# Optimization experiments

Measured on AMD Instinct MI355X. Metric: run time of the kernel, lower is better.

The kernel has to match this reference:

```python
import jax, jax.numpy as jnp
import numpy as np

SIZES = {"a": 1024, "b": 512, "c": 2048}
OUT = 1024
N_STREAMS = 3
EPS = 1e-5


def _layer_norm(x, w, b):
    mu = jnp.mean(x, axis=-1, keepdims=True)
    var = jnp.mean(jnp.square(x - mu), axis=-1, keepdims=True)
    return (x - mu) * jax.lax.rsqrt(var + EPS) * w + b


def setup_inputs() -> dict:
    key = jax.random.key(0)
    ks = iter(jax.random.split(key, 32))
    B = 32768
    inp = {}
    for name, d in SIZES.items():
        inp[f"x_{name}"] = jax.random.normal(next(ks), (B, d), dtype=jnp.float32)
        inp[f"ln_w_{name}"] = jnp.ones((d,), dtype=jnp.float32)
        inp[f"ln_b_{name}"] = jnp.zeros((d,), dtype=jnp.float32)
        inp[f"W_{name}"] = jax.random.normal(next(ks), (d, OUT), dtype=jnp.float32) / np.sqrt(d)
        inp[f"b_{name}"] = jnp.zeros((OUT,), dtype=jnp.float32)
        # gating linear: size -> n_streams * gate_size (gate_size = OUT, pointwise)
        inp[f"Wg_{name}"] = 0.005 * jax.random.normal(next(ks), (d, N_STREAMS * OUT), dtype=jnp.float32)
        inp[f"bg_{name}"] = jnp.zeros((N_STREAMS * OUT,), dtype=jnp.float32)
    return inp


def reference(x_a, ln_w_a, ln_b_a, W_a, b_a, Wg_a, bg_a,
              x_b, ln_w_b, ln_b_b, W_b, b_b, Wg_b, bg_b,
              x_c, ln_w_c, ln_b_c, W_c, b_c, Wg_c, bg_c):
    xs = [x_a, x_b, x_c]
    lns = [(ln_w_a, ln_b_a), (ln_w_b, ln_b_b), (ln_w_c, ln_b_c)]
    lins = [(W_a, b_a), (W_b, b_b), (W_c, b_c)]
    gats = [(Wg_a, bg_a), (Wg_b, bg_b), (Wg_c, bg_c)]

    gate_logits = 0.0
    outputs = []
    for x, (lw, lb), (W, b), (Wg, bg) in zip(xs, lns, lins, gats):
        f = jax.nn.relu(_layer_norm(x, lw, lb))          # [B, d]
        outputs.append(f @ W + b)                         # [B, OUT]
        gate_logits = gate_logits + (f @ Wg + bg)         # [B, 3*OUT]

    B = x_a.shape[0]
    gate = jax.nn.softmax(gate_logits.reshape(B, N_STREAMS, OUT), axis=1)  # [B,3,OUT]
    out = sum(gate[:, i] * outputs[i] for i in range(N_STREAMS))
    return out
```

## Files before the change

kernel.cpp:

```cpp
#include <hip/hip_runtime.h>
#include <hip/hip_bf16.h>
#include <stdint.h>

#define B_ROWS 32768
#define KTOT   3584
#define NC     6144
#define OUT_N  1024

typedef unsigned short ushort_t;
typedef __attribute__((ext_vector_type(8))) short bf16x8;
typedef __attribute__((ext_vector_type(4))) float f32x4;

__device__ __forceinline__ float b2f(unsigned short u) {
    union { unsigned int i; float f; } x; x.i = ((unsigned int)u) << 16; return x.f;
}
__device__ __forceinline__ unsigned short f2b(float f) {
    union { float f; unsigned int i; } x; x.f = f;
    unsigned int r = x.i + 0x7fffu + ((x.i >> 16) & 1u);
    return (unsigned short)(r >> 16);
}

__device__ __forceinline__ void gload_lds16(const void* g, void* l) {
    auto g1 = reinterpret_cast<const __attribute__((address_space(1))) char*>(
        reinterpret_cast<uintptr_t>(g));
    auto l3 = reinterpret_cast<__attribute__((address_space(3))) char*>(
        (uint32_t)reinterpret_cast<uintptr_t>(l));
    __builtin_amdgcn_global_load_lds(g1, l3, 16, 0, 0);
}

template<int OFF>
__device__ __forceinline__ bf16x8 dsr(uint32_t addr) {
    bf16x8 d;
    asm volatile("ds_read_b128 %0, %1 offset:%2" : "=v"(d) : "v"(addr), "i"(OFF));
    return d;
}

__global__ __launch_bounds__(256) void pack_wt_kernel(
    const float* __restrict__ Wa, const float* __restrict__ Wga,
    const float* __restrict__ Wb, const float* __restrict__ Wgb,
    const float* __restrict__ Wc, const float* __restrict__ Wgc,
    ushort_t* __restrict__ WT)
{
    int s = blockIdx.y;
    const float *Ws, *Wgs; int d, koff;
    if (s == 0)      { Ws = Wa; Wgs = Wga; d = 1024; koff = 0;    }
    else if (s == 1) { Ws = Wb; Wgs = Wgb; d = 512;  koff = 1024; }
    else             { Ws = Wc; Wgs = Wgc; d = 2048; koff = 1536; }
    int kt = blockIdx.x >> 6;
    int ntile = blockIdx.x & 63;
    if (kt >= (d >> 6)) return;
    int k0 = kt * 64, n0 = ntile * 64;
    const float* src; int ld, ncol0;
    if (n0 < 1024) { src = Ws;  ld = 1024; ncol0 = n0; }
    else           { src = Wgs; ld = 3072; ncol0 = n0 - 1024; }

    __shared__ float tile[64][65];
    int tx = threadIdx.x & 63, ty = threadIdx.x >> 6;
    for (int r = ty; r < 64; r += 4)
        tile[r][tx] = src[(size_t)(k0 + r) * ld + ncol0 + tx];
    __syncthreads();
    for (int r = ty; r < 64; r += 4)
        WT[(size_t)(n0 + r) * KTOT + koff + k0 + tx] = f2b(tile[tx][r]);
}

__global__ __launch_bounds__(256) void pack_bias_kernel(
    const float* __restrict__ ba, const float* __restrict__ bb, const float* __restrict__ bc,
    const float* __restrict__ bga, const float* __restrict__ bgb, const float* __restrict__ bgc,
    float* __restrict__ bias)
{
    int i = blockIdx.x * 256 + threadIdx.x;
    if (i >= NC) return;
    float v;
    if (i < 1024)      v = ba[i];
    else if (i < 2048) v = bb[i - 1024];
    else if (i < 3072) v = bc[i - 2048];
    else { int g = i - 3072; v = bga[g] + bgb[g] + bgc[g]; }
    bias[i] = v;
}

__global__ __launch_bounds__(256) void ln_relu_kernel(
    const float* __restrict__ xa, const float* __restrict__ xb, const float* __restrict__ xc,
    const float* __restrict__ wa, const float* __restrict__ wb, const float* __restrict__ wc,
    const float* __restrict__ ba, const float* __restrict__ bb, const float* __restrict__ bc,
    ushort_t* __restrict__ F)
{
    int row = blockIdx.x;
    int s = blockIdx.y;
    const float *x, *w, *b; int d, koff;
    if (s == 0)      { x = xa; w = wa; b = ba; d = 1024; koff = 0;    }
    else if (s == 1) { x = xb; w = wb; b = bb; d = 512;  koff = 1024; }
    else             { x = xc; w = wc; b = bc; d = 2048; koff = 1536; }
    const float* xr = x + (size_t)row * d;
    int tid = threadIdx.x;

    float s1 = 0.f, s2 = 0.f;
    for (int i = tid * 4; i < d; i += 1024) {
        float4 v = *(const float4*)(xr + i);
        s1 += v.x + v.y + v.z + v.w;
        s2 += v.x * v.x + v.y * v.y + v.z * v.z + v.w * v.w;
    }
    for (int o = 32; o > 0; o >>= 1) {
        s1 += __shfl_down(s1, o, 64);
        s2 += __shfl_down(s2, o, 64);
    }
    __shared__ float red1[4], red2[4], bcast[2];
    int wv = tid >> 6, ln = tid & 63;
    if (ln == 0) { red1[wv] = s1; red2[wv] = s2; }
    __syncthreads();
    if (tid == 0) {
        float t1 = red1[0] + red1[1] + red1[2] + red1[3];
        float t2 = red2[0] + red2[1] + red2[2] + red2[3];
        float mean = t1 / d;
        float var = t2 / d - mean * mean;
        bcast[0] = mean;
        bcast[1] = rsqrtf(var + 1e-5f);
    }
    __syncthreads();
    float mean = bcast[0], rstd = bcast[1];

    ushort_t* Fr = F + (size_t)row * KTOT + koff;
    for (int i = tid * 4; i < d; i += 1024) {
        float4 v  = *(const float4*)(xr + i);
        float4 wv4 = *(const float4*)(w + i);
        float4 bv4 = *(const float4*)(b + i);
        float o0 = fmaxf(0.f, (v.x - mean) * rstd * wv4.x + bv4.x);
        float o1 = fmaxf(0.f, (v.y - mean) * rstd * wv4.y + bv4.y);
        float o2 = fmaxf(0.f, (v.z - mean) * rstd * wv4.z + bv4.z);
        float o3 = fmaxf(0.f, (v.w - mean) * rstd * wv4.w + bv4.w);
        union { ushort_t u[4]; uint2 v2; } pk;
        pk.u[0] = f2b(o0); pk.u[1] = f2b(o1); pk.u[2] = f2b(o2); pk.u[3] = f2b(o3);
        *(uint2*)(Fr + i) = pk.v2;
    }
}

__global__ __launch_bounds__(512, 2) void gemm_kernel(
    const ushort_t* __restrict__ F, const ushort_t* __restrict__ WT,
    const float* __restrict__ bias, ushort_t* __restrict__ C)
{
    extern __shared__ ushort_t lds_u16[];

    int bid = blockIdx.x;
    int newid = (bid & 7) * 384 + (bid >> 3);
    int rowpanel = newid / 24;
    int j = newid % 24;
    int row0 = rowpanel * 256;
    int n0, koff, klen, c0;
    if (j < 4)       { n0 = j * 256;            koff = 0;    klen = 1024; c0 = j * 256; }
    else if (j < 8)  { n0 = (j - 4) * 256;      koff = 1024; klen = 512;  c0 = 1024 + (j - 4) * 256; }
    else if (j < 12) { n0 = (j - 8) * 256;      koff = 1536; klen = 2048; c0 = 2048 + (j - 8) * 256; }
    else             { n0 = 1024 + (j - 12) * 256; koff = 0; klen = 3584; c0 = 3072 + (j - 12) * 256; }

    int tid = threadIdx.x, w = tid >> 6, l = tid & 63;
    int wm0 = (w >> 2) * 128;
    int wn0 = (w & 3) * 64;

    int srow = w * 32 + (l >> 3);
    int scol = (((l & 7) ^ (l >> 3)) << 3);
    const ushort_t* Ag = F  + (size_t)(row0 + srow) * KTOT + koff + scol;
    const ushort_t* Bg = WT + (size_t)(n0   + srow) * KTOT + koff + scol;

    uint32_t lds_base = (uint32_t)(uintptr_t)lds_u16;
    uint32_t ldsStA = lds_base + (uint32_t)w * 4096u;

#define STG_A(SELOFF, kt, JJ0) do {                                              \
        gload_lds16(Ag + (size_t)(kt) * 64 + (size_t)(JJ0) * 8 * KTOT,           \
                    (void*)(uintptr_t)(ldsStA + (SELOFF) + (JJ0) * 1024u));      \
        gload_lds16(Ag + (size_t)(kt) * 64 + (size_t)((JJ0) + 1) * 8 * KTOT,     \
                    (void*)(uintptr_t)(ldsStA + (SELOFF) + ((JJ0) + 1) * 1024u)); } while (0)
#define STG_B(SELOFF, kt, JJ0) do {                                              \
        gload_lds16(Bg + (size_t)(kt) * 64 + (size_t)(JJ0) * 8 * KTOT,           \
                    (void*)(uintptr_t)(ldsStA + 32768u + (SELOFF) + (JJ0) * 1024u)); \
        gload_lds16(Bg + (size_t)(kt) * 64 + (size_t)((JJ0) + 1) * 8 * KTOT,     \
                    (void*)(uintptr_t)(ldsStA + 32768u + (SELOFF) + ((JJ0) + 1) * 1024u)); } while (0)

    int rl = l & 15;
    int c16_0 = ((l >> 4)    ) ^ (l & 7);
    int c16_1 = ((l >> 4) + 4) ^ (l & 7);
    uint32_t aA0 = lds_base + (uint32_t)((wm0 + rl) * 128 + c16_0 * 16);
    uint32_t aA1 = lds_base + (uint32_t)((wm0 + rl) * 128 + c16_1 * 16);
    uint32_t aB0 = lds_base + 32768u + (uint32_t)((wn0 + rl) * 128 + c16_0 * 16);
    uint32_t aB1 = lds_base + 32768u + (uint32_t)((wn0 + rl) * 128 + c16_1 * 16);

#define R_A4(dst, base, MI0) do {                          \
        dst[0] = dsr<((MI0)+0)*2048>(base);                \
        dst[1] = dsr<((MI0)+1)*2048>(base);                \
        dst[2] = dsr<((MI0)+2)*2048>(base);                \
        dst[3] = dsr<((MI0)+3)*2048>(base); } while (0)
#define R_B2(dst, base, NI0) do {                          \
        dst[0] = dsr<((NI0)+0)*2048>(base);                \
        dst[1] = dsr<((NI0)+1)*2048>(base); } while (0)

#define MFMA_Q(Aks0, Aks1, Bks0, Bks1, MI0, NI0) do {                            \
        _Pragma("unroll")                                                        \
        for (int mi = 0; mi < 4; ++mi)                                           \
            _Pragma("unroll")                                                    \
            for (int ni = 0; ni < 2; ++ni)                                       \
                acc[(MI0)+mi][(NI0)+ni] = __builtin_amdgcn_mfma_f32_16x16x32_bf16( \
                    Aks0[mi], Bks0[ni], acc[(MI0)+mi][(NI0)+ni], 0, 0, 0);       \
        _Pragma("unroll")                                                        \
        for (int mi = 0; mi < 4; ++mi)                                           \
            _Pragma("unroll")                                                    \
            for (int ni = 0; ni < 2; ++ni)                                       \
                acc[(MI0)+mi][(NI0)+ni] = __builtin_amdgcn_mfma_f32_16x16x32_bf16( \
                    Aks1[mi], Bks1[ni], acc[(MI0)+mi][(NI0)+ni], 0, 0, 0);       \
        } while (0)

    f32x4 acc[8][4];
    #pragma unroll
    for (int mi = 0; mi < 8; ++mi)
        #pragma unroll
        for (int ni = 0; ni < 4; ++ni)
            acc[mi][ni] = (f32x4){0.f, 0.f, 0.f, 0.f};

    int nkt = klen >> 6;

    STG_A(0u, 0, 0); STG_A(0u, 0, 2); STG_B(0u, 0, 0); STG_B(0u, 0, 2);
    STG_A(65536u, 1, 0);

    for (int t = 0; t < nkt; ++t) {
        const uint32_t co  = (t & 1) ? 65536u : 0u;
        const uint32_t no_ = co ^ 65536u;
        int t1 = (t + 1 < nkt) ? t + 1 : nkt - 1;
        int t2 = (t + 2 < nkt) ? t + 2 : nkt - 1;

        asm volatile("s_waitcnt vmcnt(2)" ::: "memory");
        __builtin_amdgcn_s_barrier();

        bf16x8 alo0[4], alo1[4], ahi0[4], ahi1[4];
        bf16x8 blo0[2], blo1[2], bhi0[2], bhi1[2];

        R_A4(alo0, aA0 + co, 0); R_A4(alo1, aA1 + co, 0);
        R_B2(blo0, aB0 + co, 0); R_B2(blo1, aB1 + co, 0);
        STG_A(no_, t1, 2);
        __builtin_amdgcn_s_barrier();
        asm volatile("s_waitcnt lgkmcnt(0)" ::: "memory");
        __builtin_amdgcn_sched_barrier(0);
        __builtin_amdgcn_s_setprio(1);
        MFMA_Q(alo0, alo1, blo0, blo1, 0, 0);
        __builtin_amdgcn_s_setprio(0);
        __builtin_amdgcn_s_barrier();

        R_B2(bhi0, aB0 + co, 2); R_B2(bhi1, aB1 + co, 2);
        STG_B(no_, t1, 0);
        __builtin_amdgcn_s_barrier();
        asm volatile("s_waitcnt lgkmcnt(0)" ::: "memory");
        __builtin_amdgcn_sched_barrier(0);
        __builtin_amdgcn_s_setprio(1);
        MFMA_Q(alo0, alo1, bhi0, bhi1, 0, 2);
        __builtin_amdgcn_s_setprio(0);
        __builtin_amdgcn_s_barrier();

        R_A4(ahi0, aA0 + co, 4); R_A4(ahi1, aA1 + co, 4);
        STG_B(no_, t1, 2);
        __builtin_amdgcn_s_barrier();
        asm volatile("s_waitcnt lgkmcnt(0)" ::: "memory");
        __builtin_amdgcn_sched_barrier(0);
        __builtin_amdgcn_s_setprio(1);
        MFMA_Q(ahi0, ahi1, blo0, blo1, 4, 0);
        __builtin_amdgcn_s_setprio(0);
        __builtin_amdgcn_s_barrier();

        STG_A(co, t2, 0);
        __builtin_amdgcn_s_barrier();
        __builtin_amdgcn_s_setprio(1);
        MFMA_Q(ahi0, ahi1, bhi0, bhi1, 4, 2);
        __builtin_amdgcn_s_setprio(0);
    }

#undef STG_A
#undef STG_B
#undef R_A4
#undef R_B2
#undef MFMA_Q

    #pragma unroll
    for (int ni = 0; ni < 4; ++ni) {
        int col = c0 + wn0 + ni * 16 + rl;
        float bv = bias[col];
        #pragma unroll
        for (int mi = 0; mi < 8; ++mi) {
            int rbase = row0 + wm0 + mi * 16 + (l >> 4) * 4;
            #pragma unroll
            for (int r = 0; r < 4; ++r)
                C[(size_t)(rbase + r) * NC + col] = f2b(acc[mi][ni][r] + bv);
        }
    }
}

typedef __attribute__((ext_vector_type(8))) unsigned short u16x8;

__global__ __launch_bounds__(256) void fuse_kernel(
    const ushort_t* __restrict__ C, float* __restrict__ out)
{
    int t = blockIdx.x * 256 + threadIdx.x;
    int b  = t >> 7;
    int j0 = (t & 127) << 3;
    const ushort_t* Cr = C + (size_t)b * NC;
    u16x8 oa = *(const u16x8*)(Cr + j0);
    u16x8 ob = *(const u16x8*)(Cr + 1024 + j0);
    u16x8 oc = *(const u16x8*)(Cr + 2048 + j0);
    u16x8 g0 = *(const u16x8*)(Cr + 3072 + j0);
    u16x8 g1 = *(const u16x8*)(Cr + 4096 + j0);
    u16x8 g2 = *(const u16x8*)(Cr + 5120 + j0);
    float res[8];
    #pragma unroll
    for (int k = 0; k < 8; ++k) {
        float a0 = b2f(g0[k]), a1 = b2f(g1[k]), a2 = b2f(g2[k]);
        float m = fmaxf(a0, fmaxf(a1, a2));
        float e0 = __expf(a0 - m), e1 = __expf(a1 - m), e2 = __expf(a2 - m);
        float inv = 1.f / (e0 + e1 + e2);
        res[k] = (e0 * b2f(oa[k]) + e1 * b2f(ob[k]) + e2 * b2f(oc[k])) * inv;
    }
    float* op = out + (size_t)b * 1024 + j0;
    *(float4*)op       = (float4){res[0], res[1], res[2], res[3]};
    *(float4*)(op + 4) = (float4){res[4], res[5], res[6], res[7]};
}

extern "C" void kernel_launch(void* const* d_in, const int* in_sizes, int n_in,
                              void* d_out, int out_size, void* d_ws, size_t ws_size,
                              hipStream_t stream)
{
    const float* x_a   = (const float*)d_in[0];
    const float* lnw_a = (const float*)d_in[1];
    const float* lnb_a = (const float*)d_in[2];
    const float* W_a   = (const float*)d_in[3];
    const float* b_a   = (const float*)d_in[4];
    const float* Wg_a  = (const float*)d_in[5];
    const float* bg_a  = (const float*)d_in[6];
    const float* x_b   = (const float*)d_in[7];
    const float* lnw_b = (const float*)d_in[8];
    const float* lnb_b = (const float*)d_in[9];
    const float* W_b   = (const float*)d_in[10];
    const float* b_b   = (const float*)d_in[11];
    const float* Wg_b  = (const float*)d_in[12];
    const float* bg_b  = (const float*)d_in[13];
    const float* x_c   = (const float*)d_in[14];
    const float* lnw_c = (const float*)d_in[15];
    const float* lnb_c = (const float*)d_in[16];
    const float* W_c   = (const float*)d_in[17];
    const float* b_c   = (const float*)d_in[18];
    const float* Wg_c  = (const float*)d_in[19];
    const float* bg_c  = (const float*)d_in[20];

    char* ws = (char*)d_ws;
    ushort_t* F    = (ushort_t*)ws;
    ushort_t* WT   = (ushort_t*)(ws + 234881024);
    ushort_t* Cbuf = (ushort_t*)(ws + 234881024 + 29360128);
    float*    bias = (float*)   (ws + 234881024 + 29360128 + 402653184);

    hipLaunchKernelGGL(pack_wt_kernel, dim3(2048, 3), dim3(256), 0, stream,
                       W_a, Wg_a, W_b, Wg_b, W_c, Wg_c, WT);
    hipLaunchKernelGGL(pack_bias_kernel, dim3(24), dim3(256), 0, stream,
                       b_a, b_b, b_c, bg_a, bg_b, bg_c, bias);
    hipLaunchKernelGGL(ln_relu_kernel, dim3(32768, 3), dim3(256), 0, stream,
                       x_a, x_b, x_c, lnw_a, lnw_b, lnw_c, lnb_a, lnb_b, lnb_c, F);
    hipLaunchKernelGGL(gemm_kernel, dim3(3072), dim3(512), 131072, stream,
                       F, WT, bias, Cbuf);
    hipLaunchKernelGGL(fuse_kernel, dim3(16384), dim3(256), 0, stream,
                       Cbuf, (float*)d_out);
}
```

Before: 1.081 ms.

## Restructure GEMM main loop into one-barrier double buffer with interleaved LDS reads

Replaces the four-phase per-iteration schedule, which had many block barriers and staggered partial prefetches, with a simpler double-buffer scheme. The whole next K tile is issued at the top of each iteration and there is a single vmcnt(0) plus barrier at the end. LDS fragment reads are interleaved with MFMA groups using graded lgkmcnt waits, so compute can start before all fragments arrive. It also changes the block-to-tile mapping so each XCD handles a fixed set of column tiles across row panels, aiming for better L2 reuse of weights. In exchange the global-load prefetch distance drops to one tile, and the full vmcnt(0) wait each iteration may expose memory latency.

```diff
diff --git a/kernel.cpp b/kernel.cpp
--- a/kernel.cpp
+++ b/kernel.cpp
@@ -140,10 +140,15 @@
     extern __shared__ ushort_t lds_u16[];
 
     int bid = blockIdx.x;
-    int newid = (bid & 7) * 384 + (bid >> 3);
-    int rowpanel = newid / 24;
-    int j = newid % 24;
-    int row0 = rowpanel * 256;
+    int xcd = bid & 7;
+    int local = bid >> 3;
+    int rp = local / 3;
+    int jj = local - rp * 3;
+    int j;
+    if (xcd < 4) j = (jj == 0) ? xcd : (jj == 1) ? 8 + xcd : 12 + xcd;
+    else         j = (jj == 0) ? xcd : (jj == 1) ? 12 + xcd : 16 + xcd;
+
+    int row0 = rp * 256;
     int n0, koff, klen, c0;
     if (j < 4)       { n0 = j * 256;            koff = 0;    klen = 1024; c0 = j * 256; }
     else if (j < 8)  { n0 = (j - 4) * 256;      koff = 1024; klen = 512;  c0 = 1024 + (j - 4) * 256; }
@@ -181,29 +186,19 @@
     uint32_t aB0 = lds_base + 32768u + (uint32_t)((wn0 + rl) * 128 + c16_0 * 16);
     uint32_t aB1 = lds_base + 32768u + (uint32_t)((wn0 + rl) * 128 + c16_1 * 16);
 
-#define R_A4(dst, base, MI0) do {                          \
-        dst[0] = dsr<((MI0)+0)*2048>(base);                \
-        dst[1] = dsr<((MI0)+1)*2048>(base);                \
-        dst[2] = dsr<((MI0)+2)*2048>(base);                \
-        dst[3] = dsr<((MI0)+3)*2048>(base); } while (0)
-#define R_B2(dst, base, NI0) do {                          \
-        dst[0] = dsr<((NI0)+0)*2048>(base);                \
-        dst[1] = dsr<((NI0)+1)*2048>(base); } while (0)
-
-#define MFMA_Q(Aks0, Aks1, Bks0, Bks1, MI0, NI0) do {                            \
-        _Pragma("unroll")                                                        \
-        for (int mi = 0; mi < 4; ++mi)                                           \
-            _Pragma("unroll")                                                    \
-            for (int ni = 0; ni < 2; ++ni)                                       \
+#define WAITL(N) do { asm volatile("s_waitcnt lgkmcnt(" #N ")" ::: "memory");   \
+                      __builtin_amdgcn_sched_barrier(0); } while (0)
+
+#define MFMA8(AV, BV, MI0, NI0) do {                                            \
+        __builtin_amdgcn_s_setprio(1);                                          \
+        _Pragma("unroll")                                                       \
+        for (int mi = 0; mi < 4; ++mi)                                          \
+            _Pragma("unroll")                                                   \
+            for (int ni = 0; ni < 2; ++ni)                                      \
                 acc[(MI0)+mi][(NI0)+ni] = __builtin_amdgcn_mfma_f32_16x16x32_bf16( \
-                    Aks0[mi], Bks0[ni], acc[(MI0)+mi][(NI0)+ni], 0, 0, 0);       \
-        _Pragma("unroll")                                                        \
-        for (int mi = 0; mi < 4; ++mi)                                           \
-            _Pragma("unroll")                                                    \
-            for (int ni = 0; ni < 2; ++ni)                                       \
-                acc[(MI0)+mi][(NI0)+ni] = __builtin_amdgcn_mfma_f32_16x16x32_bf16( \
-                    Aks1[mi], Bks1[ni], acc[(MI0)+mi][(NI0)+ni], 0, 0, 0);       \
-        } while (0)
+                    AV[mi], BV[ni], acc[(MI0)+mi][(NI0)+ni], 0, 0, 0);          \
+        __builtin_amdgcn_s_setprio(0);                                          \
+    } while (0)
 
     f32x4 acc[8][4];
     #pragma unroll
@@ -215,63 +210,65 @@
     int nkt = klen >> 6;
 
     STG_A(0u, 0, 0); STG_A(0u, 0, 2); STG_B(0u, 0, 0); STG_B(0u, 0, 2);
-    STG_A(65536u, 1, 0);
+    asm volatile("s_waitcnt vmcnt(0)" ::: "memory");
+    __builtin_amdgcn_s_barrier();
 
     for (int t = 0; t < nkt; ++t) {
         const uint32_t co  = (t & 1) ? 65536u : 0u;
         const uint32_t no_ = co ^ 65536u;
-        int t1 = (t + 1 < nkt) ? t + 1 : nkt - 1;
-        int t2 = (t + 2 < nkt) ? t + 2 : nkt - 1;
-
-        asm volatile("s_waitcnt vmcnt(2)" ::: "memory");
-        __builtin_amdgcn_s_barrier();
+        uint32_t A0 = aA0 + co, A1 = aA1 + co, B0 = aB0 + co, B1 = aB1 + co;
+
+        if (t + 1 < nkt) {
+            STG_A(no_, t + 1, 0); STG_A(no_, t + 1, 2);
+            STG_B(no_, t + 1, 0); STG_B(no_, t + 1, 2);
+        }
 
         bf16x8 alo0[4], alo1[4], ahi0[4], ahi1[4];
         bf16x8 blo0[2], blo1[2], bhi0[2], bhi1[2];
 
-        R_A4(alo0, aA0 + co, 0); R_A4(alo1, aA1 + co, 0);
-        R_B2(blo0, aB0 + co, 0); R_B2(blo1, aB1 + co, 0);
-        STG_A(no_, t1, 2);
+        alo0[0] = dsr<0>(A0); alo0[1] = dsr<2048>(A0);
+        alo0[2] = dsr<4096>(A0); alo0[3] = dsr<6144>(A0);
+        blo0[0] = dsr<0>(B0); blo0[1] = dsr<2048>(B0);
+        bhi0[0] = dsr<4096>(B0); bhi0[1] = dsr<6144>(B0);
+        alo1[0] = dsr<0>(A1); alo1[1] = dsr<2048>(A1);
+        alo1[2] = dsr<4096>(A1); alo1[3] = dsr<6144>(A1);
+        blo1[0] = dsr<0>(B1); blo1[1] = dsr<2048>(B1);
+
+        WAITL(8);
+        MFMA8(alo0, blo0, 0, 0);
+        bhi1[0] = dsr<4096>(B1); bhi1[1] = dsr<6144>(B1);
+
+        WAITL(8);
+        MFMA8(alo0, bhi0, 0, 2);
+        ahi0[0] = dsr<8192>(A0);  ahi0[1] = dsr<10240>(A0);
+        ahi0[2] = dsr<12288>(A0); ahi0[3] = dsr<14336>(A0);
+
+        WAITL(6);
+        MFMA8(alo1, blo1, 0, 0);
+
+        WAITL(4);
+        MFMA8(alo1, bhi1, 0, 2);
+        ahi1[0] = dsr<8192>(A1);  ahi1[1] = dsr<10240>(A1);
+        ahi1[2] = dsr<12288>(A1); ahi1[3] = dsr<14336>(A1);
+
+        WAITL(4);
+        MFMA8(ahi0, blo0, 4, 0);
+
+        MFMA8(ahi0, bhi0, 4, 2);
+
+        WAITL(0);
+        MFMA8(ahi1, blo1, 4, 0);
+
+        MFMA8(ahi1, bhi1, 4, 2);
+
+        asm volatile("s_waitcnt vmcnt(0)" ::: "memory");
         __builtin_amdgcn_s_barrier();
-        asm volatile("s_waitcnt lgkmcnt(0)" ::: "memory");
-        __builtin_amdgcn_sched_barrier(0);
-        __builtin_amdgcn_s_setprio(1);
-        MFMA_Q(alo0, alo1, blo0, blo1, 0, 0);
-        __builtin_amdgcn_s_setprio(0);
-        __builtin_amdgcn_s_barrier();
-
-        R_B2(bhi0, aB0 + co, 2); R_B2(bhi1, aB1 + co, 2);
-        STG_B(no_, t1, 0);
-        __builtin_amdgcn_s_barrier();
-        asm volatile("s_waitcnt lgkmcnt(0)" ::: "memory");
-        __builtin_amdgcn_sched_barrier(0);
-        __builtin_amdgcn_s_setprio(1);
-        MFMA_Q(alo0, alo1, bhi0, bhi1, 0, 2);
-        __builtin_amdgcn_s_setprio(0);
-        __builtin_amdgcn_s_barrier();
-
-        R_A4(ahi0, aA0 + co, 4); R_A4(ahi1, aA1 + co, 4);
-        STG_B(no_, t1, 2);
-        __builtin_amdgcn_s_barrier();
-        asm volatile("s_waitcnt lgkmcnt(0)" ::: "memory");
-        __builtin_amdgcn_sched_barrier(0);
-        __builtin_amdgcn_s_setprio(1);
-        MFMA_Q(ahi0, ahi1, blo0, blo1, 4, 0);
-        __builtin_amdgcn_s_setprio(0);
-        __builtin_amdgcn_s_barrier();
-
-        STG_A(co, t2, 0);
-        __builtin_amdgcn_s_barrier();
-        __builtin_amdgcn_s_setprio(1);
-        MFMA_Q(ahi0, ahi1, bhi0, bhi1, 4, 2);
-        __builtin_amdgcn_s_setprio(0);
     }
 
 #undef STG_A
 #undef STG_B
-#undef R_A4
-#undef R_B2
-#undef MFMA_Q
+#undef WAITL
+#undef MFMA8
 
     #pragma unroll
     for (int ni = 0; ni < 4; ++ni) {
```

Measured after the change: 1.116 ms. +3.3%, slower.
